# Optimization experiments

Measured on AMD Instinct MI355X. Metric: run time of the kernel, lower is better.

The kernel has to match this reference:

```python
import jax, jax.numpy as jnp
import numpy as np

NEG = -1e30  # effective -inf, safe under logaddexp


def _rna_loss(logits, targets, fbank_len, text_len, blank=0):
    """RNA loss: forward lattice DP over (T, U).

    logits: [B, T, U, V] raw scores (U = max_labels + 1)
    targets: [B, U-1] int labels; fbank_len/text_len: [B] int lengths.
    Each frame emits exactly one symbol (blank -> stay at u, label -> u+1).
    """
    log_probs = jax.nn.log_softmax(logits, axis=-1)          # [B,T,U,V]
    B, T, U, V = logits.shape
    L = U - 1
    lab = targets.astype(jnp.int32)                          # [B,L]
    lp_blank = jnp.transpose(log_probs[..., blank], (1, 0, 2))   # [T,B,U]
    # prob of emitting label u+1 while at state u: gather target token
    lp_label = jnp.take_along_axis(
        log_probs[:, :, :L, :], lab[:, None, :, None], axis=3)[..., 0]  # [B,T,L]
    lp_label = jnp.transpose(lp_label, (1, 0, 2))            # [T,B,L]

    alpha0 = jnp.full((B, U), NEG, dtype=log_probs.dtype).at[:, 0].set(0.0)

    def step(alpha, xs):
        lpb, lpl = xs                                        # [B,U], [B,L]
        stay = alpha + lpb                                   # emit blank
        move = jnp.pad(alpha[:, :L] + lpl, ((0, 0), (1, 0)),
                       constant_values=NEG)                  # emit label
        new = jnp.logaddexp(stay, move)
        return new, new

    _, alphas = jax.lax.scan(step, alpha0, (lp_blank, lp_label))  # [T,B,U]
    alphas = jnp.concatenate([alpha0[None], alphas], axis=0)      # [T+1,B,U]
    ll = alphas[fbank_len, jnp.arange(B), text_len]               # [B]
    return -ll


def setup_inputs() -> dict:
    key = jax.random.key(0)
    k1, k2, k3, k4 = jax.random.split(key, 4)
    B, T, L, V = 4, 512, 64, 1024
    logits = jax.random.normal(k1, (B, T, L + 1, V), dtype=jnp.float32)
    targets = jax.random.randint(k2, (B, L), 1, V, dtype=jnp.int32)
    fbank_len = jax.random.randint(k3, (B,), 384, T + 1, dtype=jnp.int32)
    text_len = jax.random.randint(k4, (B,), 32, L + 1, dtype=jnp.int32)
    return {"logits": logits, "targets": targets,
            "fbank_len": fbank_len, "text_len": text_len}


def reference(logits, targets, fbank_len, text_len):
    loss = _rna_loss(logits, targets, fbank_len, text_len, blank=0)
    return loss.mean()  # reduction='mean'
```

## Files before the change

kernel.cpp:

```cpp
#include <hip/hip_runtime.h>

#define NEGF (-1e30f)

namespace {

constexpr int B = 4, T = 512, L = 64, U = 65, V = 1024;

__device__ __forceinline__ float lse2(float a, float b) {
    float m = fmaxf(a, b);
    float d = fminf(a, b) - m;
    return m + __logf(1.0f + __expf(d));
}

__device__ __forceinline__ float dpp_bcast_op_max(float x) {
    x = fmaxf(x, __int_as_float(__builtin_amdgcn_update_dpp(0, __float_as_int(x), 0xB1, 0xF, 0xF, true)));
    x = fmaxf(x, __int_as_float(__builtin_amdgcn_update_dpp(0, __float_as_int(x), 0x4E, 0xF, 0xF, true)));
    x = fmaxf(x, __int_as_float(__builtin_amdgcn_update_dpp(0, __float_as_int(x), 0x141, 0xF, 0xF, true)));
    x = fmaxf(x, __int_as_float(__builtin_amdgcn_update_dpp(0, __float_as_int(x), 0x140, 0xF, 0xF, true)));
    x = fmaxf(x, __shfl_xor(x, 16, 64));
    x = fmaxf(x, __shfl_xor(x, 32, 64));
    return x;
}
__device__ __forceinline__ float dpp_bcast_op_sum(float x) {
    x += __int_as_float(__builtin_amdgcn_update_dpp(0, __float_as_int(x), 0xB1, 0xF, 0xF, true));
    x += __int_as_float(__builtin_amdgcn_update_dpp(0, __float_as_int(x), 0x4E, 0xF, 0xF, true));
    x += __int_as_float(__builtin_amdgcn_update_dpp(0, __float_as_int(x), 0x141, 0xF, 0xF, true));
    x += __int_as_float(__builtin_amdgcn_update_dpp(0, __float_as_int(x), 0x140, 0xF, 0xF, true));
    x += __shfl_xor(x, 16, 64);
    x += __shfl_xor(x, 32, 64);
    return x;
}

__device__ __forceinline__ float dpp_shr1(float x) {
    return __int_as_float(__builtin_amdgcn_update_dpp(
        0, __float_as_int(x), 0x138, 0xF, 0xF, true));
}

__global__ __launch_bounds__(256) void rna_lse_kernel(
    const float* __restrict__ logits, const int* __restrict__ targets,
    const int* __restrict__ fbank_len, const int* __restrict__ text_len,
    float* __restrict__ lpb, float* __restrict__ lpl) {
    const int lane = threadIdx.x & 63;
    const int row  = blockIdx.x * 4 + (threadIdx.x >> 6);
    const int u  = row % U;
    const int bt = row / U;
    const int t  = bt % T;
    const int b  = bt / T;

    const int fb = fbank_len[b];
    const int tl = text_len[b];
    if (t >= fb || u > tl || u > t + 1 || (tl - u) > (fb - t)) return;

    const float*  p  = logits + (size_t)row * V;
    const float4* p4 = (const float4*)p;
    float4 v0 = p4[lane];
    float4 v1 = p4[lane + 64];
    float4 v2 = p4[lane + 128];
    float4 v3 = p4[lane + 192];

    float m = fmaxf(fmaxf(fmaxf(v0.x, v0.y), fmaxf(v0.z, v0.w)),
              fmaxf(fmaxf(fmaxf(v1.x, v1.y), fmaxf(v1.z, v1.w)),
              fmaxf(fmaxf(fmaxf(v2.x, v2.y), fmaxf(v2.z, v2.w)),
                    fmaxf(fmaxf(v3.x, v3.y), fmaxf(v3.z, v3.w)))));
    m = dpp_bcast_op_max(m);

    float s = __expf(v0.x - m) + __expf(v0.y - m) + __expf(v0.z - m) + __expf(v0.w - m)
            + __expf(v1.x - m) + __expf(v1.y - m) + __expf(v1.z - m) + __expf(v1.w - m)
            + __expf(v2.x - m) + __expf(v2.y - m) + __expf(v2.z - m) + __expf(v2.w - m)
            + __expf(v3.x - m) + __expf(v3.y - m) + __expf(v3.z - m) + __expf(v3.w - m);
    s = dpp_bcast_op_sum(s);

    if (lane == 0) {
        float lse = m + __logf(s);
        lpb[(b * U + u) * T + t] = v0.x - lse;
        if (u < L) {
            int tgt = targets[b * L + u];
            lpl[(b * U + u + 1) * T + t] = p[tgt] - lse;
        }
    }
}

__global__ __launch_bounds__(64, 1) void rna_dp_kernel(
    const float* __restrict__ lpb, const float* __restrict__ lpl,
    const int* __restrict__ fbank_len, const int* __restrict__ text_len,
    float* __restrict__ partial) {
    const int lane = threadIdx.x;
    const int b    = blockIdx.x;
    const int fb   = fbank_len[b];
    const int tl   = text_len[b];

    const float* pbR   = lpb + (b * U + lane) * T;
    const float* plR   = lpl + (b * U + lane) * T;
    const float* pbR64 = lpb + (b * U + 64) * T;
    const float* plR64 = lpl + (b * U + 64) * T;

    float alpha   = (lane == 0) ? 0.0f : NEGF;
    float alpha64 = NEGF;

    constexpr int G = 32;
    float cb[G], cl[G], cb64[G], cl64[G];
#pragma unroll
    for (int q = 0; q < G / 4; ++q) {
        float4 a  = *(const float4*)(pbR   + 4 * q);
        float4 c  = *(const float4*)(plR   + 4 * q);
        float4 e  = *(const float4*)(pbR64 + 4 * q);
        float4 g4 = *(const float4*)(plR64 + 4 * q);
        cb[4*q+0]=a.x;  cb[4*q+1]=a.y;  cb[4*q+2]=a.z;  cb[4*q+3]=a.w;
        cl[4*q+0]=c.x;  cl[4*q+1]=c.y;  cl[4*q+2]=c.z;  cl[4*q+3]=c.w;
        cb64[4*q+0]=e.x;  cb64[4*q+1]=e.y;  cb64[4*q+2]=e.z;  cb64[4*q+3]=e.w;
        cl64[4*q+0]=g4.x; cl64[4*q+1]=g4.y; cl64[4*q+2]=g4.z; cl64[4*q+3]=g4.w;
    }

    const int nFull = fb / G;
    for (int g = 0; g < nFull; ++g) {
        const int t0 = g * G;
        float nb[G], nl[G], nb64[G], nl64[G];
        const bool pf = (g + 1 < nFull);
        if (pf) {
            const int tn = t0 + G;
#pragma unroll
            for (int q = 0; q < G / 4; ++q) {
                float4 a  = *(const float4*)(pbR   + tn + 4 * q);
                float4 c  = *(const float4*)(plR   + tn + 4 * q);
                float4 e  = *(const float4*)(pbR64 + tn + 4 * q);
                float4 g4 = *(const float4*)(plR64 + tn + 4 * q);
                nb[4*q+0]=a.x;  nb[4*q+1]=a.y;  nb[4*q+2]=a.z;  nb[4*q+3]=a.w;
                nl[4*q+0]=c.x;  nl[4*q+1]=c.y;  nl[4*q+2]=c.z;  nl[4*q+3]=c.w;
                nb64[4*q+0]=e.x;  nb64[4*q+1]=e.y;  nb64[4*q+2]=e.z;  nb64[4*q+3]=e.w;
                nl64[4*q+0]=g4.x; nl64[4*q+1]=g4.y; nl64[4*q+2]=g4.z; nl64[4*q+3]=g4.w;
            }
        }
#pragma unroll
        for (int j = 0; j < G; ++j) {
            const int t = t0 + j;
            float ap   = dpp_shr1(alpha);
            float stay = alpha + cb[j];
            float move = (lane == 0) ? NEGF : (ap + cl[j]);
            float na   = lse2(stay, move);
            float stay64 = alpha64 + cb64[j];
            float move64 = alpha + cl64[j];
            alpha64 = lse2(stay64, move64);
            alpha   = na;
            if (lane > t + 1) alpha = NEGF;
            if (t + 1 < 64)   alpha64 = NEGF;
        }
        if (pf) {
#pragma unroll
            for (int j = 0; j < G; ++j) {
                cb[j] = nb[j]; cl[j] = nl[j]; cb64[j] = nb64[j]; cl64[j] = nl64[j];
            }
        }
    }

    for (int t = nFull * G; t < fb; ++t) {
        float bj  = pbR[t];
        float lj  = plR[t];
        float b64 = pbR64[t];
        float l64 = plR64[t];
        float ap   = dpp_shr1(alpha);
        float stay = alpha + bj;
        float move = (lane == 0) ? NEGF : (ap + lj);
        float na   = lse2(stay, move);
        float stay64 = alpha64 + b64;
        float move64 = alpha + l64;
        alpha64 = lse2(stay64, move64);
        alpha   = na;
        if (lane > t + 1) alpha = NEGF;
        if (t + 1 < 64)   alpha64 = NEGF;
    }

    float ans = (tl < 64) ? __shfl(alpha, tl, 64) : __shfl(alpha64, 63, 64);
    if (lane == 0) partial[b] = ans;
}

__global__ void rna_sum_kernel(const float* __restrict__ partial,
                               float* __restrict__ out) {
    out[0] = -(partial[0] + partial[1] + partial[2] + partial[3]) * (1.0f / B);
}

}

extern "C" void kernel_launch(void* const* d_in, const int* in_sizes, int n_in,
                              void* d_out, int out_size, void* d_ws, size_t ws_size,
                              hipStream_t stream) {
    const float* logits  = (const float*)d_in[0];
    const int*   targets = (const int*)d_in[1];
    const int*   fbl     = (const int*)d_in[2];
    const int*   txl     = (const int*)d_in[3];
    float* lpb     = (float*)d_ws;
    float* lpl     = lpb + (size_t)B * U * T;
    float* partial = lpl + (size_t)B * U * T;
    float* out     = (float*)d_out;

    const int rows = B * T * U;
    rna_lse_kernel<<<rows / 4, 256, 0, stream>>>(logits, targets, fbl, txl, lpb, lpl);
    rna_dp_kernel<<<B, 64, 0, stream>>>(lpb, lpl, fbl, txl, partial);
    rna_sum_kernel<<<1, 1, 0, stream>>>(partial, out);
}
```

Measured before the change: 717.5 us.

## Make LSE kernel persistent grid-stride with software-pipelined row prefetch

The log-softmax kernel now runs a fixed grid of 2048 blocks, and each wave loops over rows with a stride. The next valid row's logits are loaded before the previous row is reduced, so memory latency overlaps with compute. Lengths are loaded once into registers, and the target logit is pulled from registers with a shuffle instead of a second global read. This removes per-row launch and wave overhead and the dependent gather load. In exchange it adds register pressure and uneven work across waves, since rows that fail the length mask are skipped.

```diff
diff --git a/kernel.cpp b/kernel.cpp
--- a/kernel.cpp
+++ b/kernel.cpp
@@ -30,7 +30,6 @@
     x += __shfl_xor(x, 32, 64);
     return x;
 }
-
 __device__ __forceinline__ float dpp_shr1(float x) {
     return __int_as_float(__builtin_amdgcn_update_dpp(
         0, __float_as_int(x), 0x138, 0xF, 0xF, true));
@@ -41,43 +40,67 @@
     const int* __restrict__ fbank_len, const int* __restrict__ text_len,
     float* __restrict__ lpb, float* __restrict__ lpl) {
     const int lane = threadIdx.x & 63;
-    const int row  = blockIdx.x * 4 + (threadIdx.x >> 6);
-    const int u  = row % U;
-    const int bt = row / U;
-    const int t  = bt % T;
-    const int b  = bt / T;
-
-    const int fb = fbank_len[b];
-    const int tl = text_len[b];
-    if (t >= fb || u > tl || u > t + 1 || (tl - u) > (fb - t)) return;
-
-    const float*  p  = logits + (size_t)row * V;
-    const float4* p4 = (const float4*)p;
-    float4 v0 = p4[lane];
-    float4 v1 = p4[lane + 64];
-    float4 v2 = p4[lane + 128];
-    float4 v3 = p4[lane + 192];
-
-    float m = fmaxf(fmaxf(fmaxf(v0.x, v0.y), fmaxf(v0.z, v0.w)),
-              fmaxf(fmaxf(fmaxf(v1.x, v1.y), fmaxf(v1.z, v1.w)),
-              fmaxf(fmaxf(fmaxf(v2.x, v2.y), fmaxf(v2.z, v2.w)),
-                    fmaxf(fmaxf(v3.x, v3.y), fmaxf(v3.z, v3.w)))));
-    m = dpp_bcast_op_max(m);
-
-    float s = __expf(v0.x - m) + __expf(v0.y - m) + __expf(v0.z - m) + __expf(v0.w - m)
-            + __expf(v1.x - m) + __expf(v1.y - m) + __expf(v1.z - m) + __expf(v1.w - m)
-            + __expf(v2.x - m) + __expf(v2.y - m) + __expf(v2.z - m) + __expf(v2.w - m)
-            + __expf(v3.x - m) + __expf(v3.y - m) + __expf(v3.z - m) + __expf(v3.w - m);
-    s = dpp_bcast_op_sum(s);
-
-    if (lane == 0) {
+    const int wid  = blockIdx.x * 4 + (threadIdx.x >> 6);
+    const int nw   = gridDim.x * 4;
+    constexpr int TOTAL = B * T * U;
+
+    const int f0 = fbank_len[0], f1 = fbank_len[1], f2 = fbank_len[2], f3 = fbank_len[3];
+    const int x0 = text_len[0],  x1 = text_len[1],  x2 = text_len[2],  x3 = text_len[3];
+
+    bool   have = false;
+    int    pu = 0, pt = 0, pb = 0;
+    float4 c0, c1, c2, c3;
+
+    auto reduce_store = [&](void) {
+        float m = fmaxf(fmaxf(fmaxf(c0.x, c0.y), fmaxf(c0.z, c0.w)),
+                  fmaxf(fmaxf(fmaxf(c1.x, c1.y), fmaxf(c1.z, c1.w)),
+                  fmaxf(fmaxf(fmaxf(c2.x, c2.y), fmaxf(c2.z, c2.w)),
+                        fmaxf(fmaxf(c3.x, c3.y), fmaxf(c3.z, c3.w)))));
+        m = dpp_bcast_op_max(m);
+        float s = __expf(c0.x - m) + __expf(c0.y - m) + __expf(c0.z - m) + __expf(c0.w - m)
+                + __expf(c1.x - m) + __expf(c1.y - m) + __expf(c1.z - m) + __expf(c1.w - m)
+                + __expf(c2.x - m) + __expf(c2.y - m) + __expf(c2.z - m) + __expf(c2.w - m)
+                + __expf(c3.x - m) + __expf(c3.y - m) + __expf(c3.z - m) + __expf(c3.w - m);
+        s = dpp_bcast_op_sum(s);
         float lse = m + __logf(s);
-        lpb[(b * U + u) * T + t] = v0.x - lse;
-        if (u < L) {
-            int tgt = targets[b * L + u];
-            lpl[(b * U + u + 1) * T + t] = p[tgt] - lse;
-        }
-    }
+
+        if (pu < L) {
+            int tgt  = targets[pb * L + pu];
+            int blk  = tgt >> 8;
+            int lsrc = (tgt >> 2) & 63;
+            int comp = tgt & 3;
+            float4 vb = (blk == 0) ? c0 : (blk == 1) ? c1 : (blk == 2) ? c2 : c3;
+            float  el = (comp == 0) ? vb.x : (comp == 1) ? vb.y : (comp == 2) ? vb.z : vb.w;
+            float  ptgt = __shfl(el, lsrc, 64);
+            if (lane == 0)
+                lpl[(pb * U + pu + 1) * T + pt] = ptgt - lse;
+        }
+        if (lane == 0)
+            lpb[(pb * U + pu) * T + pt] = c0.x - lse;
+    };
+
+    for (int row = wid; row < TOTAL; row += nw) {
+        const int u  = row % U;
+        const int bt = row / U;
+        const int t  = bt & (T - 1);
+        const int b  = bt >> 9;
+        const int fb = (b == 0) ? f0 : (b == 1) ? f1 : (b == 2) ? f2 : f3;
+        const int tl = (b == 0) ? x0 : (b == 1) ? x1 : (b == 2) ? x2 : x3;
+        if (t >= fb || u > tl || u > t + 1 || (tl - u) > (fb - t)) continue;
+
+        const float4* p4 = (const float4*)(logits + (size_t)row * V);
+        float4 n0 = p4[lane];
+        float4 n1 = p4[lane + 64];
+        float4 n2 = p4[lane + 128];
+        float4 n3 = p4[lane + 192];
+
+        if (have) reduce_store();
+
+        c0 = n0; c1 = n1; c2 = n2; c3 = n3;
+        pu = u; pt = t; pb = b;
+        have = true;
+    }
+    if (have) reduce_store();
 }
 
 __global__ __launch_bounds__(64, 1) void rna_dp_kernel(
@@ -192,8 +215,7 @@
     float* partial = lpl + (size_t)B * U * T;
     float* out     = (float*)d_out;
 
-    const int rows = B * T * U;
-    rna_lse_kernel<<<rows / 4, 256, 0, stream>>>(logits, targets, fbl, txl, lpb, lpl);
+    rna_lse_kernel<<<2048, 256, 0, stream>>>(logits, targets, fbl, txl, lpb, lpl);
     rna_dp_kernel<<<B, 64, 0, stream>>>(lpb, lpl, fbl, txl, partial);
     rna_sum_kernel<<<1, 1, 0, stream>>>(partial, out);
 }
```

Result: slower. 741.6 us (+3.4%).
